# Performance work log

Hardware: AMD Instinct MI355X
Metric: run time of the kernel (lower is better)

Reference implementation:

```python
import jax, jax.numpy as jnp
import numpy as np

CONF_THRES = 0.25
IOU_THRES = 0.45
MAX_ANCHORS = 50
PRE_NMS_TOPK = 2048   # candidate cap, standard fused-NMS trick to bound the IoU matrix
NEG = -1.0e9
NUM_CLASSES = 80
IMG = 640.0


def setup_inputs() -> dict:
    key = jax.random.key(0)
    k1, k2, k3, k4 = jax.random.split(key, 4)
    B, N = 16, 25200
    # realistic xyxy boxes inside a 640x640 image
    cxcy = jax.random.uniform(k1, (B, N, 2), minval=0.0, maxval=IMG)
    wh = jax.random.uniform(k2, (B, N, 2), minval=4.0, maxval=64.0)
    x1y1 = jnp.clip(cxcy - 0.5 * wh, 0.0, IMG)
    x2y2 = jnp.clip(cxcy + 0.5 * wh, 0.0, IMG)
    conf = jax.random.uniform(k3, (B, N, 1))
    cls = jax.random.randint(k4, (B, N, 1), 0, NUM_CLASSES).astype(jnp.float32)
    x = jnp.concatenate([x1y1, x2y2, conf, cls], axis=-1)  # [B, N, 6]
    return {"x": x}


def _box_iou_matrix(boxes):
    # boxes: [K, 4] xyxy -> [K, K] pairwise IoU
    x1, y1, x2, y2 = boxes[:, 0], boxes[:, 1], boxes[:, 2], boxes[:, 3]
    area = jnp.maximum(x2 - x1, 0.0) * jnp.maximum(y2 - y1, 0.0)  # [K]
    iw = jnp.maximum(jnp.minimum(x2[:, None], x2[None, :]) - jnp.maximum(x1[:, None], x1[None, :]), 0.0)
    ih = jnp.maximum(jnp.minimum(y2[:, None], y2[None, :]) - jnp.maximum(y1[:, None], y1[None, :]), 0.0)
    inter = iw * ih
    union = area[:, None] + area[None, :] - inter
    return inter / jnp.maximum(union, 1e-9)


def _nms_single(bx):
    # bx: [N, 6] -> [MAX_ANCHORS, 6], rows padded with -1 (keep_shape semantics)
    scores = bx[:, 4]
    s = jnp.where(scores > CONF_THRES, scores, NEG)  # confidence filter
    top_s, top_i = jax.lax.top_k(s, PRE_NMS_TOPK)     # sort descending by score
    cand = jnp.take(bx, top_i, axis=0)                # [K, 6]
    cvalid = top_s > 0.5 * NEG                        # passed conf filter

    iou = _box_iou_matrix(cand[:, :4])                # [K, K]
    idxs = jnp.arange(PRE_NMS_TOPK)
    # box i may only suppress lower-scored boxes j > i
    suppr_rows = (iou >= IOU_THRES) & (idxs[None, :] > idxs[:, None])

    def step(suppressed, i):
        keep_i = cvalid[i] & jnp.logical_not(suppressed[i])
        suppressed = suppressed | (keep_i & suppr_rows[i])
        return suppressed, keep_i

    _, keep = jax.lax.scan(step, jnp.zeros(PRE_NMS_TOPK, dtype=bool), idxs)

    final_s = jnp.where(keep, cand[:, 4], NEG)
    sel_s, sel_i = jax.lax.top_k(final_s, MAX_ANCHORS)  # top-50 kept boxes by conf
    rows = jnp.take(cand, sel_i, axis=0)                # [50, 6]
    return jnp.where((sel_s > 0.5 * NEG)[:, None], rows, -1.0)


def reference(x):
    # x: [B, N, 6] -> [B, MAX_ANCHORS, 6]
    return jax.vmap(_nms_single)(x)
```

## Files before the change

kernel.cpp:

```cpp
#include <hip/hip_runtime.h>

#define BATCH   16
#define NANCH   25200
#define TPB     512
#define NWAVES  (TPB / 64)
#define MAXK    50
#define PRETOPK 2048
#define CONF_T  0.25f
#define IOU_T   0.45f
#define NEGV    -1000000000.0f
#define T0      0.9905f
#define CAP     320
#define SPLIT   32
#define K1B     256
#define PERBLK  788
#define SCAP    96

__device__ __forceinline__ unsigned long long make_key(float s, int idx) {
    return ((unsigned long long)__float_as_uint(s) << 32) |
           (unsigned long long)(65535 - idx);
}

__global__ __launch_bounds__(K1B) void collect_kernel(const float* __restrict__ x,
                                                      unsigned long long* __restrict__ skeys,
                                                      unsigned int* __restrict__ scnt) {
    __shared__ unsigned long long l_keys[SCAP];
    __shared__ int l_cnt;
    const int b    = blockIdx.x >> 5;
    const int s    = blockIdx.x & 31;
    const int base = s * PERBLK;
    const int end  = (base + PERBLK < NANCH) ? base + PERBLK : NANCH;
    const float* __restrict__ xb = x + (size_t)b * NANCH * 6;

    if (threadIdx.x == 0) l_cnt = 0;
    __syncthreads();

    #pragma unroll
    for (int k = 0; k < 4; ++k) {
        const int i = base + (int)threadIdx.x + k * K1B;
        if (i < end) {
            const float v = xb[(size_t)i * 6 + 4];
            if (v > T0) {
                int slot = atomicAdd(&l_cnt, 1);
                if (slot < SCAP) l_keys[slot] = make_key(v, i);
            }
        }
    }
    __syncthreads();

    const int c = l_cnt;
    if (threadIdx.x == 0) scnt[blockIdx.x] = (unsigned)c;
    const int cc = c < SCAP ? c : SCAP;
    for (int j = (int)threadIdx.x; j < cc; j += K1B)
        skeys[(size_t)blockIdx.x * SCAP + j] = l_keys[j];
}

__global__ __launch_bounds__(TPB, 1) void nms_kernel(const float* __restrict__ x,
                                                     const unsigned long long* __restrict__ skeys,
                                                     const unsigned int* __restrict__ scnt,
                                                     float* __restrict__ out) {
    __shared__ float s_scores[NANCH];
    __shared__ __align__(16) unsigned long long s_keys[CAP];
    __shared__ float s_srows[CAP][8];
    __shared__ float s_kx1[MAXK], s_ky1[MAXK], s_kx2[MAXK], s_ky2[MAXK], s_ka[MAXK];
    __shared__ float s_wval[NWAVES];
    __shared__ int   s_widx[NWAVES];
    __shared__ int   s_slc[SPLIT], s_soff[SPLIT];
    __shared__ int   s_cnt, s_bad, s_nk, s_best;

    const int b    = blockIdx.x;
    const int tid  = threadIdx.x;
    const int lane = tid & 63;
    const int wave = tid >> 6;

    const float* __restrict__ xb = x + (size_t)b * NANCH * 6;
    float* __restrict__ ob       = out + (size_t)b * MAXK * 6;

    if (tid < CAP) s_keys[tid] = 0ULL;
    if (tid < SPLIT) s_slc[tid] = scnt ? (int)scnt[b * SPLIT + tid] : SCAP + 1;
    if (tid == 0) s_nk = 0;
    __syncthreads();
    if (tid == 0) {
        int off = 0, bad = 0;
        #pragma unroll
        for (int s = 0; s < SPLIT; ++s) {
            s_soff[s] = off;
            off += s_slc[s];
            bad |= (s_slc[s] > SCAP);
        }
        s_cnt = off;
        s_bad = bad | (off > CAP);
    }
    __syncthreads();

    const bool fast = !s_bad;
    const int  cnt  = fast ? s_cnt : 0;

    if (fast) {
        {
            const int s = tid >> 4, j0 = tid & 15;
            const int c = s_slc[s], o = s_soff[s];
            for (int j = j0; j < c; j += 16)
                s_keys[o + j] = skeys[(size_t)(b * SPLIT + s) * SCAP + j];
        }
        __syncthreads();

        if (tid < CAP) {
            const unsigned long long mykey = s_keys[tid];
            float2 r0, r1, r2;
            const bool real = tid < cnt;
            if (real) {
                int myi = 65535 - (int)(mykey & 0xFFFFULL);
                const float2* rp = (const float2*)(xb + (size_t)myi * 6);
                r0 = rp[0]; r1 = rp[1]; r2 = rp[2];
            }
            int r = 0;
            const ulonglong2* kp = (const ulonglong2*)s_keys;
            #pragma unroll 4
            for (int j = 0; j < CAP / 2; ++j) {
                const ulonglong2 p = kp[j];
                r += (p.x > mykey) ? 1 : 0;
                r += (p.y > mykey) ? 1 : 0;
            }
            if (real) {
                s_srows[r][0] = r0.x; s_srows[r][1] = r0.y;
                s_srows[r][2] = r1.x; s_srows[r][3] = r1.y;
                s_srows[r][4] = r2.x; s_srows[r][5] = r2.y;
            }
        }
        __syncthreads();

        if (wave == 0) {
            int nk = 0;
            for (int tb = 0; tb < cnt && nk < MAXK; tb += 64) {
                const int lim = (cnt - tb) < 64 ? (cnt - tb) : 64;
                float4 bx = {0.f, 0.f, 0.f, 0.f};
                float2 be = {0.f, 0.f};
                bool sup = lane >= lim;
                if (!sup) {
                    bx = *(const float4*)&s_srows[tb + lane][0];
                    be = *(const float2*)&s_srows[tb + lane][4];
                }
                const float ba = fmaxf(bx.z - bx.x, 0.f) * fmaxf(bx.w - bx.y, 0.f);

                for (int j = 0; j < nk; ++j) {
                    float iw = fmaxf(fminf(bx.z, s_kx2[j]) - fmaxf(bx.x, s_kx1[j]), 0.f);
                    float ih = fmaxf(fminf(bx.w, s_ky2[j]) - fmaxf(bx.y, s_ky1[j]), 0.f);
                    float inter = iw * ih;
                    sup = sup || (inter / fmaxf(ba + s_ka[j] - inter, 1e-9f)) >= IOU_T;
                }

                unsigned long long m = 0ULL;
                #pragma unroll 8
                for (int j = 0; j < 64; ++j) {
                    if (j >= lim) break;
                    const float4 oj = *(const float4*)&s_srows[tb + j][0];
                    const float oa = fmaxf(oj.z - oj.x, 0.f) * fmaxf(oj.w - oj.y, 0.f);
                    float iw = fmaxf(fminf(bx.z, oj.z) - fmaxf(bx.x, oj.x), 0.f);
                    float ih = fmaxf(fminf(bx.w, oj.w) - fmaxf(bx.y, oj.y), 0.f);
                    float inter = iw * ih;
                    bool ov = (inter / fmaxf(ba + oa - inter, 1e-9f)) >= IOU_T;
                    m |= ov ? (1ULL << j) : 0ULL;
                }
                m &= ~(1ULL << lane);

                unsigned long long alive = __ballot(!sup);
                unsigned long long keepmask = 0ULL;
                while (alive != 0ULL && nk < MAXK) {
                    const int j = __builtin_ctzll(alive);
                    keepmask |= 1ULL << j;
                    ++nk;
                    const unsigned long long kill = __ballot((m >> j) & 1ULL);
                    alive &= ~(kill | (1ULL << j));
                }

                if ((keepmask >> lane) & 1ULL) {
                    const int nk0 = nk - __popcll(keepmask);
                    const int pos = nk0 + __popcll(keepmask & ((1ULL << lane) - 1ULL));
                    s_kx1[pos] = bx.x; s_ky1[pos] = bx.y;
                    s_kx2[pos] = bx.z; s_ky2[pos] = bx.w; s_ka[pos] = ba;
                    ob[pos * 6 + 0] = bx.x;
                    ob[pos * 6 + 1] = bx.y;
                    ob[pos * 6 + 2] = bx.z;
                    ob[pos * 6 + 3] = bx.w;
                    ob[pos * 6 + 4] = be.x;
                    ob[pos * 6 + 5] = be.y;
                }
            }
            if (lane == 0) s_nk = nk;
        }
        __syncthreads();
    }

    const bool need_fb = !fast || (s_nk < MAXK);
    if (need_fb) {
        for (int i = tid; i < NANCH; i += TPB) {
            float sc = xb[(size_t)i * 6 + 4];
            bool dead = (sc <= CONF_T) || (fast && sc > T0);
            s_scores[i] = dead ? NEGV : sc;
        }
        __syncthreads();

        const int budget = fast ? (PRETOPK - cnt) : PRETOPK;
        int nk = s_nk;
        for (int pop = 0; pop < budget && nk < MAXK; ++pop) {
            float bv = NEGV - 1.0f;
            int   bi = NANCH;
            for (int i = tid; i < NANCH; i += TPB) {
                float sc = s_scores[i];
                if (sc > bv) { bv = sc; bi = i; }
            }
            #pragma unroll
            for (int off = 32; off >= 1; off >>= 1) {
                float ov = __shfl_down(bv, off);
                int   oi = __shfl_down(bi, off);
                if (ov > bv || (ov == bv && oi < bi)) { bv = ov; bi = oi; }
            }
            if (lane == 0) { s_wval[wave] = bv; s_widx[wave] = bi; }
            __syncthreads();
            if (wave == 0) {
                bv = (lane < NWAVES) ? s_wval[lane] : (NEGV - 1.0f);
                bi = (lane < NWAVES) ? s_widx[lane] : NANCH;
                #pragma unroll
                for (int off = 32; off >= 1; off >>= 1) {
                    float ov = __shfl_down(bv, off);
                    int   oi = __shfl_down(bi, off);
                    if (ov > bv || (ov == bv && oi < bi)) { bv = ov; bi = oi; }
                }
                if (lane == 0) {
                    s_best = (bv > 0.5f * NEGV) ? bi : -1;
                    if (s_best >= 0) s_scores[bi] = NEGV - 1.0f;
                }
            }
            __syncthreads();
            const int best = s_best;
            if (best < 0) break;

            if (wave == 0) {
                const float bx1 = xb[(size_t)best * 6 + 0];
                const float by1 = xb[(size_t)best * 6 + 1];
                const float bx2 = xb[(size_t)best * 6 + 2];
                const float by2 = xb[(size_t)best * 6 + 3];
                const float ba  = fmaxf(bx2 - bx1, 0.0f) * fmaxf(by2 - by1, 0.0f);
                bool sup = false;
                if (lane < nk) {
                    float iw = fmaxf(fminf(bx2, s_kx2[lane]) - fmaxf(bx1, s_kx1[lane]), 0.f);
                    float ih = fmaxf(fminf(by2, s_ky2[lane]) - fmaxf(by1, s_ky1[lane]), 0.f);
                    float inter = iw * ih;
                    float uni   = ba + s_ka[lane] - inter;
                    sup = (inter / fmaxf(uni, 1e-9f)) >= IOU_T;
                }
                if (lane == 0 && __ballot(sup) == 0ULL) {
                    s_kx1[nk] = bx1; s_ky1[nk] = by1;
                    s_kx2[nk] = bx2; s_ky2[nk] = by2; s_ka[nk] = ba;
                    ob[nk * 6 + 0] = bx1;
                    ob[nk * 6 + 1] = by1;
                    ob[nk * 6 + 2] = bx2;
                    ob[nk * 6 + 3] = by2;
                    ob[nk * 6 + 4] = xb[(size_t)best * 6 + 4];
                    ob[nk * 6 + 5] = xb[(size_t)best * 6 + 5];
                    s_nk = nk + 1;
                }
            }
            __syncthreads();
            nk = s_nk;
        }
        __syncthreads();
    }

    const int nkf = s_nk;
    for (int i = tid; i < (MAXK - nkf) * 6; i += TPB) {
        ob[nkf * 6 + i] = -1.0f;
    }
}

extern "C" void kernel_launch(void* const* d_in, const int* in_sizes, int n_in,
                              void* d_out, int out_size, void* d_ws, size_t ws_size,
                              hipStream_t stream) {
    const float* x = (const float*)d_in[0];
    float* out     = (float*)d_out;

    const size_t key_off   = 4096;
    const size_t key_bytes = (size_t)BATCH * SPLIT * SCAP * sizeof(unsigned long long);
    if (d_ws != nullptr && ws_size >= key_off + key_bytes) {
        unsigned int* scnt        = (unsigned int*)d_ws;
        unsigned long long* skeys = (unsigned long long*)((char*)d_ws + key_off);
        collect_kernel<<<BATCH * SPLIT, K1B, 0, stream>>>(x, skeys, scnt);
        nms_kernel<<<BATCH, TPB, 0, stream>>>(x, skeys, scnt, out);
    } else {
        nms_kernel<<<BATCH, TPB, 0, stream>>>(x, nullptr, nullptr, out);
    }
}
```

Baseline: 25.54 us.

## Fuse collect and NMS into one cooperative kernel with a grid sync

Replaces the two launches (collect, then per-batch NMS) with a single cooperative kernel. Collector blocks gather high-score candidate keys and also write the score column to a global workspace, then the whole grid syncs and the last 16 blocks run NMS. Collector blocks grow to 512 threads with 16 splits per batch instead of 32. The slow fallback now scans the global score copy instead of building a 100KB shared array, which frees LDS. This trades the second launch's gap for grid-sync cost plus an extra global store of every score, and it keeps the old two-kernel path in case the cooperative launch fails.

```diff
diff --git a/kernel.cpp b/kernel.cpp
--- a/kernel.cpp
+++ b/kernel.cpp
@@ -1,83 +1,88 @@
 #include <hip/hip_runtime.h>
-
-#define BATCH   16
-#define NANCH   25200
-#define TPB     512
-#define NWAVES  (TPB / 64)
-#define MAXK    50
-#define PRETOPK 2048
-#define CONF_T  0.25f
-#define IOU_T   0.45f
-#define NEGV    -1000000000.0f
-#define T0      0.9905f
-#define CAP     320
-#define SPLIT   32
-#define K1B     256
-#define PERBLK  788
-#define SCAP    96
+#include <hip/hip_cooperative_groups.h>
+
+namespace cg = cooperative_groups;
+
+#define BATCH    16
+#define NANCH    25200
+#define TPB      512
+#define NWAVES   (TPB / 64)
+#define MAXK     50
+#define PRETOPK  2048
+#define CONF_T   0.25f
+#define IOU_T    0.45f
+#define NEGV     -1000000000.0f
+#define T0       0.9905f
+#define CAP      320
+#define SPLIT    16
+#define PERBLK   1575
+#define SCAP     128
+#define NCOLLECT (BATCH * SPLIT)
+#define GRID     (NCOLLECT + BATCH)
 
 __device__ __forceinline__ unsigned long long make_key(float s, int idx) {
     return ((unsigned long long)__float_as_uint(s) << 32) |
            (unsigned long long)(65535 - idx);
 }
 
-__global__ __launch_bounds__(K1B) void collect_kernel(const float* __restrict__ x,
-                                                      unsigned long long* __restrict__ skeys,
-                                                      unsigned int* __restrict__ scnt) {
+__global__ __launch_bounds__(TPB, 1) void fused_kernel(
+        const float* __restrict__ x,
+        unsigned long long* __restrict__ skeys,
+        unsigned int* __restrict__ scnt,
+        float* __restrict__ gscores,
+        float* __restrict__ out) {
     __shared__ unsigned long long l_keys[SCAP];
-    __shared__ int l_cnt;
-    const int b    = blockIdx.x >> 5;
-    const int s    = blockIdx.x & 31;
-    const int base = s * PERBLK;
-    const int end  = (base + PERBLK < NANCH) ? base + PERBLK : NANCH;
-    const float* __restrict__ xb = x + (size_t)b * NANCH * 6;
-
-    if (threadIdx.x == 0) l_cnt = 0;
-    __syncthreads();
-
-    #pragma unroll
-    for (int k = 0; k < 4; ++k) {
-        const int i = base + (int)threadIdx.x + k * K1B;
-        if (i < end) {
-            const float v = xb[(size_t)i * 6 + 4];
-            if (v > T0) {
-                int slot = atomicAdd(&l_cnt, 1);
-                if (slot < SCAP) l_keys[slot] = make_key(v, i);
-            }
-        }
-    }
-    __syncthreads();
-
-    const int c = l_cnt;
-    if (threadIdx.x == 0) scnt[blockIdx.x] = (unsigned)c;
-    const int cc = c < SCAP ? c : SCAP;
-    for (int j = (int)threadIdx.x; j < cc; j += K1B)
-        skeys[(size_t)blockIdx.x * SCAP + j] = l_keys[j];
-}
-
-__global__ __launch_bounds__(TPB, 1) void nms_kernel(const float* __restrict__ x,
-                                                     const unsigned long long* __restrict__ skeys,
-                                                     const unsigned int* __restrict__ scnt,
-                                                     float* __restrict__ out) {
-    __shared__ float s_scores[NANCH];
     __shared__ __align__(16) unsigned long long s_keys[CAP];
     __shared__ float s_srows[CAP][8];
     __shared__ float s_kx1[MAXK], s_ky1[MAXK], s_kx2[MAXK], s_ky2[MAXK], s_ka[MAXK];
     __shared__ float s_wval[NWAVES];
     __shared__ int   s_widx[NWAVES];
     __shared__ int   s_slc[SPLIT], s_soff[SPLIT];
-    __shared__ int   s_cnt, s_bad, s_nk, s_best;
-
-    const int b    = blockIdx.x;
+    __shared__ int   s_lcnt, s_cnt, s_bad, s_nk, s_best;
+
+    const int bid  = blockIdx.x;
     const int tid  = threadIdx.x;
     const int lane = tid & 63;
     const int wave = tid >> 6;
 
+    if (bid < NCOLLECT) {
+        const int cb   = bid >> 4;
+        const int cs   = bid & 15;
+        const int base = cs * PERBLK;
+        const float* __restrict__ cxb = x + (size_t)cb * NANCH * 6;
+        float* __restrict__ gs        = gscores + (size_t)cb * NANCH;
+
+        if (tid == 0) s_lcnt = 0;
+        __syncthreads();
+        #pragma unroll
+        for (int k = 0; k < 4; ++k) {
+            const int i = base + tid + k * TPB;
+            if (i < base + PERBLK) {
+                const float v = cxb[(size_t)i * 6 + 4];
+                gs[i] = v;
+                if (v > T0) {
+                    int slot = atomicAdd(&s_lcnt, 1);
+                    if (slot < SCAP) l_keys[slot] = make_key(v, i);
+                }
+            }
+        }
+        __syncthreads();
+        if (tid == 0) scnt[bid] = (unsigned)s_lcnt;
+        const int cc = s_lcnt < SCAP ? s_lcnt : SCAP;
+        for (int j = tid; j < cc; j += TPB)
+            skeys[(size_t)bid * SCAP + j] = l_keys[j];
+    }
+
+    cg::this_grid().sync();
+    if (bid < NCOLLECT) return;
+
+    const int b = bid - NCOLLECT;
     const float* __restrict__ xb = x + (size_t)b * NANCH * 6;
+    float* __restrict__ gs       = gscores + (size_t)b * NANCH;
     float* __restrict__ ob       = out + (size_t)b * MAXK * 6;
 
     if (tid < CAP) s_keys[tid] = 0ULL;
-    if (tid < SPLIT) s_slc[tid] = scnt ? (int)scnt[b * SPLIT + tid] : SCAP + 1;
+    if (tid < SPLIT) s_slc[tid] = (int)scnt[b * SPLIT + tid];
     if (tid == 0) s_nk = 0;
     __syncthreads();
     if (tid == 0) {
@@ -98,9 +103,9 @@
 
     if (fast) {
         {
-            const int s = tid >> 4, j0 = tid & 15;
+            const int s = tid >> 5, j0 = tid & 31;
             const int c = s_slc[s], o = s_soff[s];
-            for (int j = j0; j < c; j += 16)
+            for (int j = j0; j < c; j += 32)
                 s_keys[o + j] = skeys[(size_t)(b * SPLIT + s) * SCAP + j];
         }
         __syncthreads();
@@ -192,23 +197,17 @@
         __syncthreads();
     }
 
-    const bool need_fb = !fast || (s_nk < MAXK);
-    if (need_fb) {
-        for (int i = tid; i < NANCH; i += TPB) {
-            float sc = xb[(size_t)i * 6 + 4];
-            bool dead = (sc <= CONF_T) || (fast && sc > T0);
-            s_scores[i] = dead ? NEGV : sc;
-        }
-        __syncthreads();
-
+    if (!fast || s_nk < MAXK) {
         const int budget = fast ? (PRETOPK - cnt) : PRETOPK;
         int nk = s_nk;
         for (int pop = 0; pop < budget && nk < MAXK; ++pop) {
             float bv = NEGV - 1.0f;
             int   bi = NANCH;
             for (int i = tid; i < NANCH; i += TPB) {
-                float sc = s_scores[i];
-                if (sc > bv) { bv = sc; bi = i; }
+                float sc = gs[i];
+                bool dead = (sc <= CONF_T) || (fast && sc > T0);
+                float v = dead ? NEGV : sc;
+                if (v > bv) { bv = v; bi = i; }
             }
             #pragma unroll
             for (int off = 32; off >= 1; off >>= 1) {
@@ -229,7 +228,7 @@
                 }
                 if (lane == 0) {
                     s_best = (bv > 0.5f * NEGV) ? bi : -1;
-                    if (s_best >= 0) s_scores[bi] = NEGV - 1.0f;
+                    if (s_best >= 0) gs[bi] = NEGV;
                 }
             }
             __syncthreads();
@@ -274,18 +273,273 @@
     }
 }
 
+__global__ __launch_bounds__(TPB) void collect_kernel(const float* __restrict__ x,
+                                                      unsigned long long* __restrict__ skeys,
+                                                      unsigned int* __restrict__ scnt) {
+    __shared__ unsigned long long l_keys[SCAP];
+    __shared__ int l_cnt;
+    const int b    = blockIdx.x >> 4;
+    const int s    = blockIdx.x & 15;
+    const int base = s * PERBLK;
+    const float* __restrict__ xb = x + (size_t)b * NANCH * 6;
+
+    if (threadIdx.x == 0) l_cnt = 0;
+    __syncthreads();
+    #pragma unroll
+    for (int k = 0; k < 4; ++k) {
+        const int i = base + (int)threadIdx.x + k * TPB;
+        if (i < base + PERBLK) {
+            const float v = xb[(size_t)i * 6 + 4];
+            if (v > T0) {
+                int slot = atomicAdd(&l_cnt, 1);
+                if (slot < SCAP) l_keys[slot] = make_key(v, i);
+            }
+        }
+    }
+    __syncthreads();
+    const int c = l_cnt;
+    if (threadIdx.x == 0) scnt[blockIdx.x] = (unsigned)c;
+    const int cc = c < SCAP ? c : SCAP;
+    for (int j = (int)threadIdx.x; j < cc; j += TPB)
+        skeys[(size_t)blockIdx.x * SCAP + j] = l_keys[j];
+}
+
+__global__ __launch_bounds__(TPB, 1) void nms_kernel(const float* __restrict__ x,
+                                                     const unsigned long long* __restrict__ skeys,
+                                                     const unsigned int* __restrict__ scnt,
+                                                     float* __restrict__ out) {
+    __shared__ float s_scores[NANCH];
+    __shared__ __align__(16) unsigned long long s_keys[CAP];
+    __shared__ float s_srows[CAP][8];
+    __shared__ float s_kx1[MAXK], s_ky1[MAXK], s_kx2[MAXK], s_ky2[MAXK], s_ka[MAXK];
+    __shared__ float s_wval[NWAVES];
+    __shared__ int   s_widx[NWAVES];
+    __shared__ int   s_slc[SPLIT], s_soff[SPLIT];
+    __shared__ int   s_cnt, s_bad, s_nk, s_best;
+
+    const int b    = blockIdx.x;
+    const int tid  = threadIdx.x;
+    const int lane = tid & 63;
+    const int wave = tid >> 6;
+
+    const float* __restrict__ xb = x + (size_t)b * NANCH * 6;
+    float* __restrict__ ob       = out + (size_t)b * MAXK * 6;
+
+    if (tid < CAP) s_keys[tid] = 0ULL;
+    if (tid < SPLIT) s_slc[tid] = scnt ? (int)scnt[b * SPLIT + tid] : SCAP + 1;
+    if (tid == 0) s_nk = 0;
+    __syncthreads();
+    if (tid == 0) {
+        int off = 0, bad = 0;
+        #pragma unroll
+        for (int s = 0; s < SPLIT; ++s) {
+            s_soff[s] = off;
+            off += s_slc[s];
+            bad |= (s_slc[s] > SCAP);
+        }
+        s_cnt = off;
+        s_bad = bad | (off > CAP);
+    }
+    __syncthreads();
+
+    const bool fast = !s_bad;
+    const int  cnt  = fast ? s_cnt : 0;
+
+    if (fast) {
+        {
+            const int s = tid >> 5, j0 = tid & 31;
+            const int c = s_slc[s], o = s_soff[s];
+            for (int j = j0; j < c; j += 32)
+                s_keys[o + j] = skeys[(size_t)(b * SPLIT + s) * SCAP + j];
+        }
+        __syncthreads();
+
+        if (tid < CAP) {
+            const unsigned long long mykey = s_keys[tid];
+            float2 r0, r1, r2;
+            const bool real = tid < cnt;
+            if (real) {
+                int myi = 65535 - (int)(mykey & 0xFFFFULL);
+                const float2* rp = (const float2*)(xb + (size_t)myi * 6);
+                r0 = rp[0]; r1 = rp[1]; r2 = rp[2];
+            }
+            int r = 0;
+            const ulonglong2* kp = (const ulonglong2*)s_keys;
+            #pragma unroll 4
+            for (int j = 0; j < CAP / 2; ++j) {
+                const ulonglong2 p = kp[j];
+                r += (p.x > mykey) ? 1 : 0;
+                r += (p.y > mykey) ? 1 : 0;
+            }
+            if (real) {
+                s_srows[r][0] = r0.x; s_srows[r][1] = r0.y;
+                s_srows[r][2] = r1.x; s_srows[r][3] = r1.y;
+                s_srows[r][4] = r2.x; s_srows[r][5] = r2.y;
+            }
+        }
+        __syncthreads();
+
+        if (wave == 0) {
+            int nk = 0;
+            for (int tb = 0; tb < cnt && nk < MAXK; tb += 64) {
+                const int lim = (cnt - tb) < 64 ? (cnt - tb) : 64;
+                float4 bx = {0.f, 0.f, 0.f, 0.f};
+                float2 be = {0.f, 0.f};
+                bool sup = lane >= lim;
+                if (!sup) {
+                    bx = *(const float4*)&s_srows[tb + lane][0];
+                    be = *(const float2*)&s_srows[tb + lane][4];
+                }
+                const float ba = fmaxf(bx.z - bx.x, 0.f) * fmaxf(bx.w - bx.y, 0.f);
+                for (int j = 0; j < nk; ++j) {
+                    float iw = fmaxf(fminf(bx.z, s_kx2[j]) - fmaxf(bx.x, s_kx1[j]), 0.f);
+                    float ih = fmaxf(fminf(bx.w, s_ky2[j]) - fmaxf(bx.y, s_ky1[j]), 0.f);
+                    float inter = iw * ih;
+                    sup = sup || (inter / fmaxf(ba + s_ka[j] - inter, 1e-9f)) >= IOU_T;
+                }
+                unsigned long long m = 0ULL;
+                #pragma unroll 8
+                for (int j = 0; j < 64; ++j) {
+                    if (j >= lim) break;
+                    const float4 oj = *(const float4*)&s_srows[tb + j][0];
+                    const float oa = fmaxf(oj.z - oj.x, 0.f) * fmaxf(oj.w - oj.y, 0.f);
+                    float iw = fmaxf(fminf(bx.z, oj.z) - fmaxf(bx.x, oj.x), 0.f);
+                    float ih = fmaxf(fminf(bx.w, oj.w) - fmaxf(bx.y, oj.y), 0.f);
+                    float inter = iw * ih;
+                    bool ov = (inter / fmaxf(ba + oa - inter, 1e-9f)) >= IOU_T;
+                    m |= ov ? (1ULL << j) : 0ULL;
+                }
+                m &= ~(1ULL << lane);
+                unsigned long long alive = __ballot(!sup);
+                unsigned long long keepmask = 0ULL;
+                while (alive != 0ULL && nk < MAXK) {
+                    const int j = __builtin_ctzll(alive);
+                    keepmask |= 1ULL << j;
+                    ++nk;
+                    const unsigned long long kill = __ballot((m >> j) & 1ULL);
+                    alive &= ~(kill | (1ULL << j));
+                }
+                if ((keepmask >> lane) & 1ULL) {
+                    const int nk0 = nk - __popcll(keepmask);
+                    const int pos = nk0 + __popcll(keepmask & ((1ULL << lane) - 1ULL));
+                    s_kx1[pos] = bx.x; s_ky1[pos] = bx.y;
+                    s_kx2[pos] = bx.z; s_ky2[pos] = bx.w; s_ka[pos] = ba;
+                    ob[pos * 6 + 0] = bx.x;
+                    ob[pos * 6 + 1] = bx.y;
+                    ob[pos * 6 + 2] = bx.z;
+                    ob[pos * 6 + 3] = bx.w;
+                    ob[pos * 6 + 4] = be.x;
+                    ob[pos * 6 + 5] = be.y;
+                }
+            }
+            if (lane == 0) s_nk = nk;
+        }
+        __syncthreads();
+    }
+
+    if (!fast || s_nk < MAXK) {
+        for (int i = tid; i < NANCH; i += TPB) {
+            float sc = xb[(size_t)i * 6 + 4];
+            bool dead = (sc <= CONF_T) || (fast && sc > T0);
+            s_scores[i] = dead ? NEGV : sc;
+        }
+        __syncthreads();
+
+        const int budget = fast ? (PRETOPK - cnt) : PRETOPK;
+        int nk = s_nk;
+        for (int pop = 0; pop < budget && nk < MAXK; ++pop) {
+            float bv = NEGV - 1.0f;
+            int   bi = NANCH;
+            for (int i = tid; i < NANCH; i += TPB) {
+                float sc = s_scores[i];
+                if (sc > bv) { bv = sc; bi = i; }
+            }
+            #pragma unroll
+            for (int off = 32; off >= 1; off >>= 1) {
+                float ov = __shfl_down(bv, off);
+                int   oi = __shfl_down(bi, off);
+                if (ov > bv || (ov == bv && oi < bi)) { bv = ov; bi = oi; }
+            }
+            if (lane == 0) { s_wval[wave] = bv; s_widx[wave] = bi; }
+            __syncthreads();
+            if (wave == 0) {
+                bv = (lane < NWAVES) ? s_wval[lane] : (NEGV - 1.0f);
+                bi = (lane < NWAVES) ? s_widx[lane] : NANCH;
+                #pragma unroll
+                for (int off = 32; off >= 1; off >>= 1) {
+                    float ov = __shfl_down(bv, off);
+                    int   oi = __shfl_down(bi, off);
+                    if (ov > bv || (ov == bv && oi < bi)) { bv = ov; bi = oi; }
+                }
+                if (lane == 0) {
+                    s_best = (bv > 0.5f * NEGV) ? bi : -1;
+                    if (s_best >= 0) s_scores[bi] = NEGV - 1.0f;
+                }
+            }
+            __syncthreads();
+            const int best = s_best;
+            if (best < 0) break;
+
+            if (wave == 0) {
+                const float bx1 = xb[(size_t)best * 6 + 0];
+                const float by1 = xb[(size_t)best * 6 + 1];
+                const float bx2 = xb[(size_t)best * 6 + 2];
+                const float by2 = xb[(size_t)best * 6 + 3];
+                const float ba  = fmaxf(bx2 - bx1, 0.0f) * fmaxf(by2 - by1, 0.0f);
+                bool sup = false;
+                if (lane < nk) {
+                    float iw = fmaxf(fminf(bx2, s_kx2[lane]) - fmaxf(bx1, s_kx1[lane]), 0.f);
+                    float ih = fmaxf(fminf(by2, s_ky2[lane]) - fmaxf(by1, s_ky1[lane]), 0.f);
+                    float inter = iw * ih;
+                    float uni   = ba + s_ka[lane] - inter;
+                    sup = (inter / fmaxf(uni, 1e-9f)) >= IOU_T;
+                }
+                if (lane == 0 && __ballot(sup) == 0ULL) {
+                    s_kx1[nk] = bx1; s_ky1[nk] = by1;
+                    s_kx2[nk] = bx2; s_ky2[nk] = by2; s_ka[nk] = ba;
+                    ob[nk * 6 + 0] = bx1;
+                    ob[nk * 6 + 1] = by1;
+                    ob[nk * 6 + 2] = bx2;
+                    ob[nk * 6 + 3] = by2;
+                    ob[nk * 6 + 4] = xb[(size_t)best * 6 + 4];
+                    ob[nk * 6 + 5] = xb[(size_t)best * 6 + 5];
+                    s_nk = nk + 1;
+                }
+            }
+            __syncthreads();
+            nk = s_nk;
+        }
+        __syncthreads();
+    }
+
+    const int nkf = s_nk;
+    for (int i = tid; i < (MAXK - nkf) * 6; i += TPB) {
+        ob[nkf * 6 + i] = -1.0f;
+    }
+}
+
 extern "C" void kernel_launch(void* const* d_in, const int* in_sizes, int n_in,
                               void* d_out, int out_size, void* d_ws, size_t ws_size,
                               hipStream_t stream) {
     const float* x = (const float*)d_in[0];
     float* out     = (float*)d_out;
 
-    const size_t key_off   = 4096;
-    const size_t key_bytes = (size_t)BATCH * SPLIT * SCAP * sizeof(unsigned long long);
-    if (d_ws != nullptr && ws_size >= key_off + key_bytes) {
+    const size_t key_off = 4096;
+    const size_t key_sz  = (size_t)NCOLLECT * SCAP * sizeof(unsigned long long);
+    const size_t sc_off  = key_off + key_sz;
+    const size_t sc_sz   = (size_t)BATCH * NANCH * sizeof(float);
+    if (d_ws != nullptr && ws_size >= sc_off + sc_sz) {
         unsigned int* scnt        = (unsigned int*)d_ws;
         unsigned long long* skeys = (unsigned long long*)((char*)d_ws + key_off);
-        collect_kernel<<<BATCH * SPLIT, K1B, 0, stream>>>(x, skeys, scnt);
+        float* gscores            = (float*)((char*)d_ws + sc_off);
+        void* args[] = {(void*)&x, (void*)&skeys, (void*)&scnt,
+                        (void*)&gscores, (void*)&out};
+        hipError_t e = hipLaunchCooperativeKernel((const void*)fused_kernel,
+                                                  dim3(GRID), dim3(TPB),
+                                                  args, 0, stream);
+        if (e == hipSuccess) return;
+        (void)hipGetLastError();
+        collect_kernel<<<BATCH * SPLIT, TPB, 0, stream>>>(x, skeys, scnt);
         nms_kernel<<<BATCH, TPB, 0, stream>>>(x, skeys, scnt, out);
     } else {
         nms_kernel<<<BATCH, TPB, 0, stream>>>(x, nullptr, nullptr, out);
```

Result: slower. 61.28 us (+139.9%).
